# Kernel optimization log

Measured on AMD Instinct MI355X. Metric: run time of the kernel, lower is better.

The kernel has to match this reference:

```python
import jax, jax.numpy as jnp
import numpy as np

H = 8          # num_heads
SCALE = 25.0   # attention temperature
THRESH = 0.75  # raw cosine-similarity mask threshold


def _l2n(x):
    return x / jnp.linalg.norm(x, axis=-1, keepdims=True)


def setup_inputs() -> dict:
    key = jax.random.key(0)
    ks = jax.random.split(key, 8)
    B, N, C, OUT = 1, 2048, 1024, 1024
    s = 0.02
    return {
        "x_cls": jax.random.normal(ks[0], (B, N, C), jnp.float32),
        "x_reg": jax.random.normal(ks[1], (B, N, C), jnp.float32),
        "cls_score": jax.random.uniform(ks[2], (N,), jnp.float32),
        "fg_score": jax.random.uniform(ks[3], (N,), jnp.float32),
        "W_qkv_cls": jax.random.normal(ks[4], (3 * C, C), jnp.float32) * s,
        "W_qkv_reg": jax.random.normal(ks[5], (3 * C, C), jnp.float32) * s,
        "W1": jax.random.normal(ks[6], (2 * C, 2 * C), jnp.float32) * s,
        "b1": jnp.zeros((2 * C,), jnp.float32),
        "W2": jax.random.normal(ks[7], (OUT, 4 * C), jnp.float32) * s,
        "b2": jnp.zeros((OUT,), jnp.float32),
    }


def reference(x_cls, x_reg, cls_score, fg_score, W_qkv_cls, W_qkv_reg, W1, b1, W2, b2):
    B, N, C = x_cls.shape
    d = C // H

    def split_qkv(x, W):
        # nn.Linear (no bias): x @ W.T, then [B,N,3,H,d] -> [3,B,H,N,d]
        qkv = (x @ W.T).reshape(B, N, 3, H, d).transpose(2, 0, 3, 1, 4)
        return qkv[0], qkv[1], qkv[2]

    q_cls, k_cls, v_cls = split_qkv(x_cls, W_qkv_cls)
    q_reg, k_reg, _ = split_qkv(x_reg, W_qkv_reg)

    q_cls, k_cls = _l2n(q_cls), _l2n(k_cls)
    q_reg, k_reg = _l2n(q_reg), _l2n(k_reg)
    v_cls_n = _l2n(v_cls)

    cs = cls_score.reshape(1, 1, 1, N)  # broadcast over [B,H,N,N]
    fs = fg_score.reshape(1, 1, 1, N)

    attn_cls_raw = jnp.einsum('bhnd,bhmd->bhnm', v_cls_n, v_cls_n)
    attn_cls = jax.nn.softmax(jnp.einsum('bhnd,bhmd->bhnm', q_cls, k_cls) * SCALE * cs, axis=-1)
    attn_reg = jax.nn.softmax(jnp.einsum('bhnd,bhmd->bhnm', q_reg, k_reg) * SCALE * fs, axis=-1)
    attn = (attn_reg + attn_cls) * 0.5

    x = jnp.einsum('bhnm,bhmd->bhnd', attn, v_cls).transpose(0, 2, 1, 3).reshape(B, N, C)
    x_ori = v_cls.transpose(0, 2, 1, 3).reshape(B, N, C)
    trans_cls = jnp.concatenate([x, x_ori], axis=-1)  # [B,N,2C]

    # head-averaged similarity, masked and re-normalized (batch element 0)
    sim_raw = attn_cls_raw.sum(axis=1)[0] / H          # [N,N]
    sim_mask = (sim_raw > THRESH).astype(x_cls.dtype)
    sim_attn = attn.sum(axis=1)[0] / H
    sim_round2 = jax.nn.softmax(sim_attn, axis=-1)
    masked = sim_mask * sim_round2
    sim_round2 = masked / masked.sum(axis=-1, keepdims=True)

    msa = trans_cls @ W1.T + b1                        # linear1 [B,N,2C]
    feat = msa[0]                                      # [N,2C]
    soft_sim = sim_round2 @ feat                       # [N,2C]
    ave = jnp.concatenate([soft_sim, feat], axis=-1)   # [N,4C]
    out = ave @ W2.T + b2                              # [N,OUT]
    return out
```

## Files before the change

kernel.cpp:

```cpp
#include <hip/hip_runtime.h>
#include <math.h>

#define PN 2048
#define PC 1024
#define PH 8
#define PD 128
#define PC3 3072

typedef __bf16 bf16x8 __attribute__((ext_vector_type(8)));
typedef float  f32x4  __attribute__((ext_vector_type(4)));
typedef short  s8v    __attribute__((ext_vector_type(8)));
typedef short  s4v    __attribute__((ext_vector_type(4)));

__device__ __forceinline__ short f2bf(float x) {
    unsigned u = __float_as_uint(x);
    unsigned r = (u + 0x7fffu + ((u >> 16) & 1u)) >> 16;
    return (short)r;
}
__device__ __forceinline__ float bf2f(short s) {
    return __uint_as_float(((unsigned)(unsigned short)s) << 16);
}

#define LDS_DMA(g, l) __builtin_amdgcn_global_load_lds( \
    (const __attribute__((address_space(1))) void*)(g), \
    (__attribute__((address_space(3))) void*)(l), 16, 0, 0)

__device__ __forceinline__ void stage128(const short* g, long ld, short* lds,
                                         int wave, int lrow, int lcol)
{
#pragma unroll
    for (int kc = 0; kc < 4; ++kc) {
        LDS_DMA(g + (long)lrow * ld + kc * 32 + lcol, lds + kc * 4096 + wave * 512);
        LDS_DMA(g + (long)(lrow + 64) * ld + kc * 32 + lcol,
                lds + kc * 4096 + 2048 + wave * 512);
    }
}

template<int BN, bool OBF16, bool BIAS>
__global__ __launch_bounds__(256) void mfma_gemm_k(
    const short* __restrict__ A, int lda, long zsa,
    const short* __restrict__ B, int ldb, long zsb,
    void* __restrict__ Cv, int ldc, long zsc,
    int K, float alpha, const float* __restrict__ bias)
{
    constexpr int NJ = BN / 32;
    __shared__ short As[128 * 32];
    __shared__ short Bs[BN * 32];
    const int tid = threadIdx.x;
    const int wave = tid >> 6, lane = tid & 63;
    const int lrow = tid >> 2;
    const int lcol = (tid & 3) * 8;
    const int z = blockIdx.z;
    A += (long)z * zsa;
    B += (long)z * zsb;
    const int row0 = blockIdx.y * 128, col0 = blockIdx.x * BN;
    const short* Ag = A + (long)(row0 + lrow) * lda + lcol;
    const short* Bg = B + (long)(col0 + lrow) * ldb + lcol;
    short* AsW0 = As + wave * 512;
    short* AsW1 = As + 2048 + wave * 512;
    short* BsW0 = Bs + wave * 512;
    short* BsW1 = Bs + 2048 + wave * 512;
    const int wr = (wave >> 1) * 64, wc = (wave & 1) * (BN / 2);
    const int m16 = lane & 15, q8 = (lane >> 4) * 8;

    f32x4 acc[4][NJ];
#pragma unroll
    for (int i = 0; i < 4; ++i)
#pragma unroll
        for (int j = 0; j < NJ; ++j) acc[i][j] = (f32x4){0.f, 0.f, 0.f, 0.f};

    for (int kt = 0; kt < K; kt += 32) {
        if (kt) __syncthreads();
        LDS_DMA(Ag + kt, AsW0);
        LDS_DMA(Ag + kt + 64 * (long)lda, AsW1);
        LDS_DMA(Bg + kt, BsW0);
        if (BN == 128) LDS_DMA(Bg + kt + 64 * (long)ldb, BsW1);
        __syncthreads();
        bf16x8 a[4], b[NJ];
#pragma unroll
        for (int i = 0; i < 4; ++i)
            a[i] = *(const bf16x8*)&As[(wr + i * 16 + m16) * 32 + q8];
#pragma unroll
        for (int j = 0; j < NJ; ++j)
            b[j] = *(const bf16x8*)&Bs[(wc + j * 16 + m16) * 32 + q8];
#pragma unroll
        for (int i = 0; i < 4; ++i)
#pragma unroll
            for (int j = 0; j < NJ; ++j)
                acc[i][j] = __builtin_amdgcn_mfma_f32_16x16x32_bf16(a[i], b[j], acc[i][j], 0, 0, 0);
    }

    const long cz = (long)z * zsc;
#pragma unroll
    for (int i = 0; i < 4; ++i) {
        const int r0 = row0 + wr + i * 16 + (lane >> 4) * 4;
#pragma unroll
        for (int j = 0; j < NJ; ++j) {
            const int c = col0 + wc + j * 16 + m16;
            const float bv = BIAS ? bias[c] : 0.0f;
#pragma unroll
            for (int t = 0; t < 4; ++t) {
                const float x = acc[i][j][t] * alpha + bv;
                const long off = cz + (long)(r0 + t) * ldc + c;
                if (OBF16) ((short*)Cv)[off] = f2bf(x);
                else       ((float*)Cv)[off] = x;
            }
        }
    }
}

__global__ __launch_bounds__(256) void attn_rowsum_k(
    const short* __restrict__ qkv,
    const float* __restrict__ cls_score, const float* __restrict__ fg_score,
    float* __restrict__ l_g)
{
    __shared__ short Qs[16384];
    __shared__ short Ks[16384];
    __shared__ float lsum[128][2];
    const int tid = threadIdx.x, wave = tid >> 6, lane = tid & 63;
    const int lrow = tid >> 2, lcol = (tid & 3) * 8;
    const int wr = (wave >> 1) * 64, wc = (wave & 1) * 64;
    const int m16 = lane & 15, q4 = lane >> 4, q8 = q4 * 8;
    const int row0 = blockIdx.x * 128, h = blockIdx.y;
    const int side = blockIdx.z >> 2, chunk = blockIdx.z & 3;
    const float* sc_g = side ? fg_score : cls_score;
    const short* base = qkv + (long)side * PN * PC3 + h * PD;
    const short* Kg = base + PC;
    stage128(base + (long)row0 * PC3, PC3, Qs, wave, lrow, lcol);
    stage128(Kg + (long)chunk * 4 * 128 * PC3, PC3, Ks, wave, lrow, lcol);
    __syncthreads();
    bf16x8 a[4][4];
#pragma unroll
    for (int i = 0; i < 4; ++i)
#pragma unroll
        for (int kc = 0; kc < 4; ++kc)
            a[i][kc] = *(const bf16x8*)&Qs[kc * 4096 + (wr + i * 16 + m16) * 32 + q8];
    float rs[4][4] = {};
    for (int ct = 0; ct < 4; ++ct) {
        const int ctg = chunk * 4 + ct;
        if (ct) {
            __syncthreads();
            stage128(Kg + (long)ctg * 128 * PC3, PC3, Ks, wave, lrow, lcol);
            __syncthreads();
        }
        f32x4 acc[4][4];
#pragma unroll
        for (int i = 0; i < 4; ++i)
#pragma unroll
            for (int j = 0; j < 4; ++j) acc[i][j] = (f32x4){0.f, 0.f, 0.f, 0.f};
#pragma unroll
        for (int kc = 0; kc < 4; ++kc) {
            bf16x8 b[4];
#pragma unroll
            for (int j = 0; j < 4; ++j)
                b[j] = *(const bf16x8*)&Ks[kc * 4096 + (wc + j * 16 + m16) * 32 + q8];
#pragma unroll
            for (int i = 0; i < 4; ++i)
#pragma unroll
                for (int j = 0; j < 4; ++j)
                    acc[i][j] = __builtin_amdgcn_mfma_f32_16x16x32_bf16(a[i][kc], b[j], acc[i][j], 0, 0, 0);
        }
#pragma unroll
        for (int j = 0; j < 4; ++j) {
            const float s25 = 25.0f * sc_g[ctg * 128 + wc + j * 16 + m16];
#pragma unroll
            for (int i = 0; i < 4; ++i)
#pragma unroll
                for (int t = 0; t < 4; ++t)
                    rs[i][t] += __expf(acc[i][j][t] * s25);
        }
    }
#pragma unroll
    for (int i = 0; i < 4; ++i)
#pragma unroll
        for (int t = 0; t < 4; ++t) {
            float v = rs[i][t];
            v += __shfl_xor(v, 1, 64); v += __shfl_xor(v, 2, 64);
            v += __shfl_xor(v, 4, 64); v += __shfl_xor(v, 8, 64);
            if (m16 == 0) lsum[wr + i * 16 + q4 * 4 + t][wave & 1] = v;
        }
    __syncthreads();
    if (tid < 128)
        atomicAdd(&l_g[((long)side * PH + h) * PN + row0 + tid],
                  lsum[tid][0] + lsum[tid][1]);
}

__global__ __launch_bounds__(256) void attn_combine_k(
    const short* __restrict__ qkv,
    const float* __restrict__ cls_score, const float* __restrict__ fg_score,
    const float* __restrict__ l_g,
    short* __restrict__ attn8)
{
    __shared__ short Ts[32768];
    const int tid = threadIdx.x, wave = tid >> 6, lane = tid & 63;
    const int lrow = tid >> 2, lcol = (tid & 3) * 8;
    const int wr = (wave >> 1) * 64, wc = (wave & 1) * 64;
    const int m16 = lane & 15, q4 = lane >> 4, q8 = q4 * 8;
    const int col0 = blockIdx.x * 128, row0 = blockIdx.y * 128, h = blockIdx.z;
    const long NN = (long)PN * PN;

    f32x4 comb[4][4];

#pragma unroll
    for (int s = 0; s < 2; ++s) {
        const short* bq = qkv + (long)s * PN * PC3 + h * PD;
        __syncthreads();
        stage128(bq + (long)row0 * PC3, PC3, Ts, wave, lrow, lcol);
        stage128(bq + PC + (long)col0 * PC3, PC3, Ts + 16384, wave, lrow, lcol);
        __syncthreads();

        float rl[4];
#pragma unroll
        for (int j = 0; j < 4; ++j)
            rl[j] = 0.5f / l_g[((long)s * PH + h) * PN + row0 + wr + j * 16 + m16];

        f32x4 acc[4][4];
#pragma unroll
        for (int i = 0; i < 4; ++i)
#pragma unroll
            for (int j = 0; j < 4; ++j) acc[i][j] = (f32x4){0.f, 0.f, 0.f, 0.f};
#pragma unroll
        for (int kc = 0; kc < 4; ++kc) {
            bf16x8 kf[4], qf[4];
#pragma unroll
            for (int i = 0; i < 4; ++i)
                kf[i] = *(const bf16x8*)&Ts[16384 + kc * 4096 + (wc + i * 16 + m16) * 32 + q8];
#pragma unroll
            for (int j = 0; j < 4; ++j)
                qf[j] = *(const bf16x8*)&Ts[kc * 4096 + (wr + j * 16 + m16) * 32 + q8];
#pragma unroll
            for (int i = 0; i < 4; ++i)
#pragma unroll
                for (int j = 0; j < 4; ++j)
                    acc[i][j] = __builtin_amdgcn_mfma_f32_16x16x32_bf16(kf[i], qf[j], acc[i][j], 0, 0, 0);
        }
        const float* sc_g = s ? fg_score : cls_score;
#pragma unroll
        for (int i = 0; i < 4; ++i) {
            const f32x4 sc4 = *(const f32x4*)&sc_g[col0 + wc + i * 16 + q4 * 4];
#pragma unroll
            for (int j = 0; j < 4; ++j)
#pragma unroll
                for (int t = 0; t < 4; ++t) {
                    const float e = __expf(acc[i][j][t] * (25.0f * sc4[t])) * rl[j];
                    comb[i][j][t] = s ? (comb[i][j][t] + e) : e;
                }
        }
    }
#pragma unroll
    for (int j = 0; j < 4; ++j) {
        const long rb = (long)h * NN + (long)(row0 + wr + j * 16 + m16) * PN
                      + col0 + wc + q4 * 4;
#pragma unroll
        for (int i = 0; i < 4; ++i) {
            s4v o;
#pragma unroll
            for (int t = 0; t < 4; ++t) o[t] = f2bf(comb[i][j][t]);
            *(s4v*)&attn8[rb + i * 16] = o;
        }
    }
}

__global__ __launch_bounds__(256) void f2bf6_k(
    const float* __restrict__ s0, const float* __restrict__ s1,
    const float* __restrict__ s2, const float* __restrict__ s3,
    const float* __restrict__ s4, const float* __restrict__ s5,
    short* __restrict__ dst)
{
    const int n0 = 512 * 1024, n1 = 512 * 1024, n2 = 768 * 1024,
              n3 = 768 * 1024, n4 = 1024 * 1024;
    const int i = blockIdx.x * 256 + threadIdx.x;
    const float* src;
    int j = i;
    if (j < n0) src = s0;
    else { j -= n0; if (j < n1) src = s1;
    else { j -= n1; if (j < n2) src = s2;
    else { j -= n2; if (j < n3) src = s3;
    else { j -= n3; if (j < n4) src = s4;
    else { j -= n4; src = s5; } } } } }
    float4 v = ((const float4*)src)[j];
    s4v o;
    o[0] = f2bf(v.x); o[1] = f2bf(v.y); o[2] = f2bf(v.z); o[3] = f2bf(v.w);
    ((s4v*)dst)[i] = o;
}

__global__ __launch_bounds__(256) void transpose_bf16_k(
    const short* __restrict__ src, int sld, short* __restrict__ dst, int dld)
{
    __shared__ short tl[64][72];
    const int r0 = blockIdx.y * 64, c0 = blockIdx.x * 64;
    const int tr = threadIdx.x >> 2;
    const int tc = (threadIdx.x & 3) * 16;
    const short* sp = src + (long)(r0 + tr) * sld + c0 + tc;
    s8v v0 = *(const s8v*)sp;
    s8v v1 = *(const s8v*)(sp + 8);
    *(s8v*)&tl[tr][tc] = v0;
    *(s8v*)&tl[tr][tc + 8] = v1;
    __syncthreads();
    s8v o0, o1;
#pragma unroll
    for (int k = 0; k < 8; ++k) { o0[k] = tl[tc + k][tr]; o1[k] = tl[tc + 8 + k][tr]; }
    short* dp = dst + (long)(c0 + tr) * dld + r0 + tc;
    *(s8v*)dp = o0;
    *(s8v*)(dp + 8) = o1;
}

__global__ __launch_bounds__(256) void norms_k(short* __restrict__ qkv,
                                               short* __restrict__ Vn,
                                               short* __restrict__ trans)
{
    const int n = blockIdx.x, which = blockIdx.y, t = threadIdx.x;
    if (which < 4) {
        short* p = qkv + (long)(which >> 1) * ((long)PN * PC3)
                 + (long)n * PC3 + (which & 1) * PC + t * 4;
        s4v v = *(s4v*)p;
        float f0 = bf2f(v[0]), f1 = bf2f(v[1]), f2 = bf2f(v[2]), f3 = bf2f(v[3]);
        float ss = f0 * f0 + f1 * f1 + f2 * f2 + f3 * f3;
        ss += __shfl_xor(ss, 16, 64); ss += __shfl_xor(ss, 8, 64);
        ss += __shfl_xor(ss, 4, 64);  ss += __shfl_xor(ss, 2, 64);
        ss += __shfl_xor(ss, 1, 64);
        const float rn = rsqrtf(ss);
        s4v o;
        o[0] = f2bf(f0 * rn); o[1] = f2bf(f1 * rn);
        o[2] = f2bf(f2 * rn); o[3] = f2bf(f3 * rn);
        *(s4v*)p = o;
    } else {
        const short* p = qkv + (long)n * PC3 + 2 * PC + t * 4;
        s4v v = *(const s4v*)p;
        float f0 = bf2f(v[0]), f1 = bf2f(v[1]), f2 = bf2f(v[2]), f3 = bf2f(v[3]);
        float ss = f0 * f0 + f1 * f1 + f2 * f2 + f3 * f3;
        ss += __shfl_xor(ss, 16, 64); ss += __shfl_xor(ss, 8, 64);
        ss += __shfl_xor(ss, 4, 64);  ss += __shfl_xor(ss, 2, 64);
        ss += __shfl_xor(ss, 1, 64);
        const float rn = rsqrtf(ss);
        s4v o;
        o[0] = f2bf(f0 * rn); o[1] = f2bf(f1 * rn);
        o[2] = f2bf(f2 * rn); o[3] = f2bf(f3 * rn);
        *(s4v*)(Vn + (long)n * PC + t * 4) = o;
        *(s4v*)(trans + (long)n * (2 * PC) + PC + t * 4) = v;
    }
}

__device__ __forceinline__ float wave_sum(float v) {
#pragma unroll
    for (int o = 32; o > 0; o >>= 1) v += __shfl_xor(v, o, 64);
    return v;
}
__device__ __forceinline__ float wave_max(float v) {
#pragma unroll
    for (int o = 32; o > 0; o >>= 1) v = fmaxf(v, __shfl_xor(v, o, 64));
    return v;
}
__device__ __forceinline__ float block_sum(float v, float* sm) {
    v = wave_sum(v);
    __syncthreads();
    if ((threadIdx.x & 63) == 0) sm[threadIdx.x >> 6] = v;
    __syncthreads();
    return sm[0] + sm[1] + sm[2] + sm[3];
}
__device__ __forceinline__ float block_max(float v, float* sm) {
    v = wave_max(v);
    __syncthreads();
    if ((threadIdx.x & 63) == 0) sm[threadIdx.x >> 6] = v;
    __syncthreads();
    return fmaxf(fmaxf(sm[0], sm[1]), fmaxf(sm[2], sm[3]));
}

__global__ __launch_bounds__(256) void sim_round2_k(
    const short* __restrict__ attn8, const short* __restrict__ Sraw,
    short* __restrict__ Sout)
{
    __shared__ float sm[4];
    const long NN = (long)PN * PN;
    const long rowoff = (long)blockIdx.x * PN + threadIdx.x * 8;
    float v[8] = {0.f, 0.f, 0.f, 0.f, 0.f, 0.f, 0.f, 0.f};
#pragma unroll
    for (int h = 0; h < PH; ++h) {
        s8v a = *(const s8v*)&attn8[(long)h * NN + rowoff];
#pragma unroll
        for (int j = 0; j < 8; ++j) v[j] += bf2f(a[j]);
    }
    bool keep[8];
    {
        s8v raw = *(const s8v*)&Sraw[rowoff];
#pragma unroll
        for (int j = 0; j < 8; ++j) {
            v[j] *= 0.125f;
            keep[j] = bf2f(raw[j]) > 0.75f;
        }
    }
    float mx = -1e30f;
#pragma unroll
    for (int j = 0; j < 8; ++j) mx = fmaxf(mx, v[j]);
    mx = block_max(mx, sm);
    float sum = 0.f;
#pragma unroll
    for (int j = 0; j < 8; ++j) { v[j] = __expf(v[j] - mx); sum += v[j]; }
    sum = block_sum(sum, sm);
    const float inv = 1.0f / sum;
    float msum = 0.f;
#pragma unroll
    for (int j = 0; j < 8; ++j) { v[j] = keep[j] ? v[j] * inv : 0.f; msum += v[j]; }
    msum = block_sum(msum, sm);
    const float minv = 1.0f / msum;
    s8v o;
#pragma unroll
    for (int j = 0; j < 8; ++j) o[j] = f2bf(v[j] * minv);
    *(s8v*)&Sout[rowoff] = o;
}

extern "C" void kernel_launch(void* const* d_in, const int* in_sizes, int n_in,
                              void* d_out, int out_size, void* d_ws, size_t ws_size,
                              hipStream_t stream)
{
    (void)in_sizes; (void)n_in; (void)out_size; (void)ws_size;
    const float* x_cls = (const float*)d_in[0];
    const float* x_reg = (const float*)d_in[1];
    const float* cls_score = (const float*)d_in[2];
    const float* fg_score = (const float*)d_in[3];
    const float* Wqc = (const float*)d_in[4];
    const float* Wqr = (const float*)d_in[5];
    const float* W1 = (const float*)d_in[6];
    const float* b1 = (const float*)d_in[7];
    const float* W2 = (const float*)d_in[8];
    const float* b2 = (const float*)d_in[9];
    float* out = (float*)d_out;

    char* w = (char*)d_ws;
    short* qkv_cls_bf = (short*)(w + ((size_t)0   << 20));
    short* qkv_reg_bf = (short*)(w + ((size_t)12  << 20));
    short* attn8      = (short*)(w + ((size_t)24  << 20));
    short* sim_bf     = (short*)(w + ((size_t)88  << 20));
    short* sim_raw_bf = (short*)(w + ((size_t)104 << 20));
    short* Vn         = (short*)(w + ((size_t)112 << 20));
    short* vT         = (short*)(w + ((size_t)116 << 20));
    short* bf_all     = (short*)(w + ((size_t)120 << 20));
    short* x_cls_bf   = bf_all;
    short* x_reg_bf   = (short*)(w + ((size_t)124 << 20));
    short* Wqc_bf     = (short*)(w + ((size_t)128 << 20));
    short* Wqr_bf     = (short*)(w + ((size_t)134 << 20));
    short* W1_bf      = (short*)(w + ((size_t)140 << 20));
    short* W2_bf      = (short*)(w + ((size_t)148 << 20));
    float* l_g        = (float*)(w + ((size_t)156 << 20));
    short* trans      = (short*)(w + ((size_t)120 << 20));
    short* featT      = (short*)(w + ((size_t)32  << 20));
    short* ave        = (short*)(w + ((size_t)40  << 20));

    const long NN = (long)PN * PN;

    f2bf6_k<<<18432, 256, 0, stream>>>(x_cls, x_reg, Wqc, Wqr, W1, W2, bf_all);

    mfma_gemm_k<128, true, false><<<dim3(24, 16, 1), 256, 0, stream>>>(
        x_cls_bf, PC, 0, Wqc_bf, PC, 0, qkv_cls_bf, PC3, 0, PC, 1.0f, nullptr);
    mfma_gemm_k<128, true, false><<<dim3(16, 16, 1), 256, 0, stream>>>(
        x_reg_bf, PC, 0, Wqr_bf, PC, 0, qkv_reg_bf, PC3, 0, PC, 1.0f, nullptr);

    norms_k<<<dim3(PN, 5), 256, 0, stream>>>(qkv_cls_bf, Vn, trans);
    transpose_bf16_k<<<dim3(PC / 64, PN / 64), 256, 0, stream>>>(
        qkv_cls_bf + 2 * PC, PC3, vT, PN);

    mfma_gemm_k<128, true, false><<<dim3(16, 16, 1), 256, 0, stream>>>(
        Vn, PC, 0, Vn, PC, 0, sim_raw_bf, PN, 0, PC, 0.125f, nullptr);

    hipMemsetAsync(l_g, 0, (size_t)2 * PH * PN * sizeof(float), stream);
    attn_rowsum_k<<<dim3(16, PH, 8), 256, 0, stream>>>(
        qkv_cls_bf, cls_score, fg_score, l_g);
    attn_combine_k<<<dim3(16, 16, PH), 256, 0, stream>>>(
        qkv_cls_bf, cls_score, fg_score, l_g, attn8);

    mfma_gemm_k<64, true, false><<<dim3(2, 16, PH), 256, 0, stream>>>(
        attn8, PN, NN, vT, PN, (long)PD * PN, trans, 2 * PC, PD, PN, 1.0f, nullptr);

    sim_round2_k<<<PN, 256, 0, stream>>>(attn8, sim_raw_bf, sim_bf);

    mfma_gemm_k<128, true, true><<<dim3(16, 16, 1), 256, 0, stream>>>(
        trans, 2 * PC, 0, W1_bf, 2 * PC, 0, ave + 2 * PC, 4 * PC, 0, 2 * PC, 1.0f, b1);

    transpose_bf16_k<<<dim3(32, 32), 256, 0, stream>>>(ave + 2 * PC, 4 * PC, featT, 2 * PC);

    mfma_gemm_k<128, true, false><<<dim3(16, 16, 1), 256, 0, stream>>>(
        sim_bf, 2 * PC, 0, featT, 2 * PC, 0, ave, 4 * PC, 0, 2 * PC, 1.0f, nullptr);

    mfma_gemm_k<64, false, true><<<dim3(16, 16, 1), 256, 0, stream>>>(
        ave, 4 * PC, 0, W2_bf, 4 * PC, 0, out, PC, 0, 4 * PC, 1.0f, b2);
}
```

Measured before the change: 514.8 us.

## Reassociate final GEMMs via W2 split and batch the two QKV projections

The tail is reassociated as sim@(feat@W2a^T) + feat@W2b^T. W2 is permuted during bf16 conversion so one GEMM produces both products transposed. The last GEMM then does the sim multiply and adds the second product plus bias in its epilogue, removing the featT transpose and the K=4096 GEMM. The two QKV projections become one z-batched launch, and the GEMM kernel gains a BM template so several GEMMs use 128x64 or 64x64 tiles for more blocks. This adds bf16 rounding of the intermediate products, and the reg batch computes the unused V third.

```diff
diff --git a/kernel.cpp b/kernel.cpp
--- a/kernel.cpp
+++ b/kernel.cpp
@@ -36,15 +36,16 @@
     }
 }
 
-template<int BN, bool OBF16, bool BIAS>
+template<int BM, int BN, bool OBF16, bool BIAS, bool ACCT>
 __global__ __launch_bounds__(256) void mfma_gemm_k(
     const short* __restrict__ A, int lda, long zsa,
     const short* __restrict__ B, int ldb, long zsb,
     void* __restrict__ Cv, int ldc, long zsc,
-    int K, float alpha, const float* __restrict__ bias)
-{
-    constexpr int NJ = BN / 32;
-    __shared__ short As[128 * 32];
+    int K, float alpha, const float* __restrict__ bias,
+    const short* __restrict__ accT, int ldat)
+{
+    constexpr int NI = BM / 32, NJ = BN / 32;
+    __shared__ short As[BM * 32];
     __shared__ short Bs[BN * 32];
     const int tid = threadIdx.x;
     const int wave = tid >> 6, lane = tid & 63;
@@ -53,38 +54,34 @@
     const int z = blockIdx.z;
     A += (long)z * zsa;
     B += (long)z * zsb;
-    const int row0 = blockIdx.y * 128, col0 = blockIdx.x * BN;
+    const int row0 = blockIdx.y * BM, col0 = blockIdx.x * BN;
     const short* Ag = A + (long)(row0 + lrow) * lda + lcol;
     const short* Bg = B + (long)(col0 + lrow) * ldb + lcol;
-    short* AsW0 = As + wave * 512;
-    short* AsW1 = As + 2048 + wave * 512;
-    short* BsW0 = Bs + wave * 512;
-    short* BsW1 = Bs + 2048 + wave * 512;
-    const int wr = (wave >> 1) * 64, wc = (wave & 1) * (BN / 2);
-    const int m16 = lane & 15, q8 = (lane >> 4) * 8;
-
-    f32x4 acc[4][NJ];
-#pragma unroll
-    for (int i = 0; i < 4; ++i)
+    const int wr = (wave >> 1) * (BM / 2), wc = (wave & 1) * (BN / 2);
+    const int m16 = lane & 15, q4 = lane >> 4, q8 = q4 * 8;
+
+    f32x4 acc[NI][NJ];
+#pragma unroll
+    for (int i = 0; i < NI; ++i)
 #pragma unroll
         for (int j = 0; j < NJ; ++j) acc[i][j] = (f32x4){0.f, 0.f, 0.f, 0.f};
 
     for (int kt = 0; kt < K; kt += 32) {
         if (kt) __syncthreads();
-        LDS_DMA(Ag + kt, AsW0);
-        LDS_DMA(Ag + kt + 64 * (long)lda, AsW1);
-        LDS_DMA(Bg + kt, BsW0);
-        if (BN == 128) LDS_DMA(Bg + kt + 64 * (long)ldb, BsW1);
+        LDS_DMA(Ag + kt, As + wave * 512);
+        if (BM == 128) LDS_DMA(Ag + kt + 64 * (long)lda, As + 2048 + wave * 512);
+        LDS_DMA(Bg + kt, Bs + wave * 512);
+        if (BN == 128) LDS_DMA(Bg + kt + 64 * (long)ldb, Bs + 2048 + wave * 512);
         __syncthreads();
-        bf16x8 a[4], b[NJ];
-#pragma unroll
-        for (int i = 0; i < 4; ++i)
+        bf16x8 a[NI], b[NJ];
+#pragma unroll
+        for (int i = 0; i < NI; ++i)
             a[i] = *(const bf16x8*)&As[(wr + i * 16 + m16) * 32 + q8];
 #pragma unroll
         for (int j = 0; j < NJ; ++j)
             b[j] = *(const bf16x8*)&Bs[(wc + j * 16 + m16) * 32 + q8];
 #pragma unroll
-        for (int i = 0; i < 4; ++i)
+        for (int i = 0; i < NI; ++i)
 #pragma unroll
             for (int j = 0; j < NJ; ++j)
                 acc[i][j] = __builtin_amdgcn_mfma_f32_16x16x32_bf16(a[i], b[j], acc[i][j], 0, 0, 0);
@@ -92,15 +89,18 @@
 
     const long cz = (long)z * zsc;
 #pragma unroll
-    for (int i = 0; i < 4; ++i) {
-        const int r0 = row0 + wr + i * 16 + (lane >> 4) * 4;
+    for (int i = 0; i < NI; ++i) {
+        const int r0 = row0 + wr + i * 16 + q4 * 4;
 #pragma unroll
         for (int j = 0; j < NJ; ++j) {
             const int c = col0 + wc + j * 16 + m16;
             const float bv = BIAS ? bias[c] : 0.0f;
+            s4v av;
+            if (ACCT) av = *(const s4v*)&accT[(long)c * ldat + r0];
 #pragma unroll
             for (int t = 0; t < 4; ++t) {
-                const float x = acc[i][j][t] * alpha + bv;
+                float x = acc[i][j][t] * alpha + bv;
+                if (ACCT) x += bf2f(av[t]);
                 const long off = cz + (long)(r0 + t) * ldc + c;
                 if (OBF16) ((short*)Cv)[off] = f2bf(x);
                 else       ((float*)Cv)[off] = x;
@@ -272,16 +272,25 @@
     const int i = blockIdx.x * 256 + threadIdx.x;
     const float* src;
     int j = i;
+    bool w2 = false;
     if (j < n0) src = s0;
     else { j -= n0; if (j < n1) src = s1;
     else { j -= n1; if (j < n2) src = s2;
     else { j -= n2; if (j < n3) src = s3;
     else { j -= n3; if (j < n4) src = s4;
-    else { j -= n4; src = s5; } } } } }
+    else { j -= n4; src = s5; w2 = true; } } } } }
     float4 v = ((const float4*)src)[j];
     s4v o;
     o[0] = f2bf(v.x); o[1] = f2bf(v.y); o[2] = f2bf(v.z); o[3] = f2bf(v.w);
-    ((s4v*)dst)[i] = o;
+    long oj = i;
+    if (w2) {
+        const int e = j << 2;
+        const int d = e >> 12, c = e & 4095;
+        const long pe = (c < 2048) ? ((long)d * 2048 + c)
+                                   : ((long)(1024 + d) * 2048 + (c - 2048));
+        oj = (long)(3584 * 1024) + (pe >> 2);
+    }
+    ((s4v*)dst)[oj] = o;
 }
 
 __global__ __launch_bounds__(256) void transpose_bf16_k(
@@ -436,31 +445,28 @@
     short* vT         = (short*)(w + ((size_t)116 << 20));
     short* bf_all     = (short*)(w + ((size_t)120 << 20));
     short* x_cls_bf   = bf_all;
-    short* x_reg_bf   = (short*)(w + ((size_t)124 << 20));
     short* Wqc_bf     = (short*)(w + ((size_t)128 << 20));
-    short* Wqr_bf     = (short*)(w + ((size_t)134 << 20));
     short* W1_bf      = (short*)(w + ((size_t)140 << 20));
-    short* W2_bf      = (short*)(w + ((size_t)148 << 20));
+    short* W2p_bf     = (short*)(w + ((size_t)148 << 20));
     float* l_g        = (float*)(w + ((size_t)156 << 20));
     short* trans      = (short*)(w + ((size_t)120 << 20));
-    short* featT      = (short*)(w + ((size_t)32  << 20));
-    short* ave        = (short*)(w + ((size_t)40  << 20));
+    short* feat       = (short*)(w + ((size_t)24  << 20));
+    short* UVt        = (short*)(w + ((size_t)32  << 20));
 
     const long NN = (long)PN * PN;
 
     f2bf6_k<<<18432, 256, 0, stream>>>(x_cls, x_reg, Wqc, Wqr, W1, W2, bf_all);
 
-    mfma_gemm_k<128, true, false><<<dim3(24, 16, 1), 256, 0, stream>>>(
-        x_cls_bf, PC, 0, Wqc_bf, PC, 0, qkv_cls_bf, PC3, 0, PC, 1.0f, nullptr);
-    mfma_gemm_k<128, true, false><<<dim3(16, 16, 1), 256, 0, stream>>>(
-        x_reg_bf, PC, 0, Wqr_bf, PC, 0, qkv_reg_bf, PC3, 0, PC, 1.0f, nullptr);
+    mfma_gemm_k<128, 64, true, false, false><<<dim3(48, 16, 2), 256, 0, stream>>>(
+        x_cls_bf, PC, (long)PN * PC, Wqc_bf, PC, (long)PC3 * PC,
+        qkv_cls_bf, PC3, (long)PN * PC3, PC, 1.0f, nullptr, nullptr, 0);
 
     norms_k<<<dim3(PN, 5), 256, 0, stream>>>(qkv_cls_bf, Vn, trans);
     transpose_bf16_k<<<dim3(PC / 64, PN / 64), 256, 0, stream>>>(
         qkv_cls_bf + 2 * PC, PC3, vT, PN);
 
-    mfma_gemm_k<128, true, false><<<dim3(16, 16, 1), 256, 0, stream>>>(
-        Vn, PC, 0, Vn, PC, 0, sim_raw_bf, PN, 0, PC, 0.125f, nullptr);
+    mfma_gemm_k<128, 64, true, false, false><<<dim3(32, 16, 1), 256, 0, stream>>>(
+        Vn, PC, 0, Vn, PC, 0, sim_raw_bf, PN, 0, PC, 0.125f, nullptr, nullptr, 0);
 
     hipMemsetAsync(l_g, 0, (size_t)2 * PH * PN * sizeof(float), stream);
     attn_rowsum_k<<<dim3(16, PH, 8), 256, 0, stream>>>(
@@ -468,19 +474,21 @@
     attn_combine_k<<<dim3(16, 16, PH), 256, 0, stream>>>(
         qkv_cls_bf, cls_score, fg_score, l_g, attn8);
 
-    mfma_gemm_k<64, true, false><<<dim3(2, 16, PH), 256, 0, stream>>>(
-        attn8, PN, NN, vT, PN, (long)PD * PN, trans, 2 * PC, PD, PN, 1.0f, nullptr);
+    mfma_gemm_k<64, 64, true, false, false><<<dim3(2, 32, PH), 256, 0, stream>>>(
+        attn8, PN, NN, vT, PN, (long)PD * PN, trans, 2 * PC, PD, PN, 1.0f,
+        nullptr, nullptr, 0);
 
     sim_round2_k<<<PN, 256, 0, stream>>>(attn8, sim_raw_bf, sim_bf);
 
-    mfma_gemm_k<128, true, true><<<dim3(16, 16, 1), 256, 0, stream>>>(
-        trans, 2 * PC, 0, W1_bf, 2 * PC, 0, ave + 2 * PC, 4 * PC, 0, 2 * PC, 1.0f, b1);
-
-    transpose_bf16_k<<<dim3(32, 32), 256, 0, stream>>>(ave + 2 * PC, 4 * PC, featT, 2 * PC);
-
-    mfma_gemm_k<128, true, false><<<dim3(16, 16, 1), 256, 0, stream>>>(
-        sim_bf, 2 * PC, 0, featT, 2 * PC, 0, ave, 4 * PC, 0, 2 * PC, 1.0f, nullptr);
-
-    mfma_gemm_k<64, false, true><<<dim3(16, 16, 1), 256, 0, stream>>>(
-        ave, 4 * PC, 0, W2_bf, 4 * PC, 0, out, PC, 0, 4 * PC, 1.0f, b2);
-}
+    mfma_gemm_k<128, 64, true, true, false><<<dim3(32, 16, 1), 256, 0, stream>>>(
+        trans, 2 * PC, 0, W1_bf, 2 * PC, 0, feat, 2 * PC, 0, 2 * PC, 1.0f, b1,
+        nullptr, 0);
+
+    mfma_gemm_k<128, 64, true, false, false><<<dim3(32, 16, 1), 256, 0, stream>>>(
+        W2p_bf, 2 * PC, 0, feat, 2 * PC, 0, UVt, PN, 0, 2 * PC, 1.0f, nullptr,
+        nullptr, 0);
+
+    mfma_gemm_k<128, 64, false, true, true><<<dim3(16, 16, 1), 256, 0, stream>>>(
+        sim_bf, PN, 0, UVt, PN, 0, out, PC, 0, PN, 1.0f, b2,
+        UVt + (long)PC * PN, PN);
+}
```

New measurement: 460.7 us. 1.12x faster.
